# Kernel tuning notes

Hardware: AMD Instinct MI355X
Metric: run time of the kernel (lower is better)

## Reference

```python
import jax, jax.numpy as jnp
import numpy as np

N_CLUSTERS = 64
N_GHOST = 2
EPS = 1e-12  # F.normalize eps


def setup_inputs() -> dict:
    key = jax.random.key(0)
    k1, k2, k3, k4 = jax.random.split(key, 4)
    n_utts, feat_dim, duration = 16, 256, 1500
    x = jax.random.normal(k1, (n_utts, feat_dim, duration), dtype=jnp.float32)
    centroids = jax.random.uniform(k2, (N_CLUSTERS, feat_dim), dtype=jnp.float32)
    # NetVLAD init ties linear.weight = 2*alpha*centroids(+ghosts); here independent params suffice for a math baseline
    lin_w = jax.random.normal(k3, (N_CLUSTERS + N_GHOST, feat_dim), dtype=jnp.float32)
    lin_b = jax.random.normal(k4, (N_CLUSTERS + N_GHOST,), dtype=jnp.float32)
    return {"x": x, "centroids": centroids, "lin_w": lin_w, "lin_b": lin_b}


def reference(x, centroids, lin_w, lin_b):
    # x: [u, f, t] -> [u, t, f]
    n_utts = x.shape[0]
    xt = jnp.transpose(x, (0, 2, 1))
    # soft assignments over clusters+ghosts, then drop ghost columns
    logits = jnp.einsum('utf,cf->utc', xt, lin_w) + lin_b  # [u,t,C+G]
    a = jax.nn.softmax(logits, axis=2)[..., :N_CLUSTERS]   # [u,t,C]
    # Fused NetVLAD aggregation (algebraically identical to
    # sum_t a[u,t,c] * (x[u,t,:] - centroids[c,:]) without materializing
    # the [u,t,C,f] residual tensor):
    comp = jnp.einsum('utc,utf->ucf', a, xt) - a.sum(axis=1)[..., None] * centroids  # [u,C,f]
    # intra-normalization (F.normalize p=2 over feat dim)
    comp = comp / jnp.maximum(jnp.linalg.norm(comp, axis=2, keepdims=True), EPS)
    sv = comp.reshape(n_utts, -1)  # [u, C*f]
    sv = sv / jnp.maximum(jnp.linalg.norm(sv, axis=1, keepdims=True), EPS)
    return sv
```

## Files before the change

### kernel.cpp

```cpp
#include <hip/hip_runtime.h>
#include <math.h>


#define NU 16
#define NF 256
#define NT 1500
#define NC 64
#define NCG 66
#define EPSN 1e-12f
#define TCH 48
#define NCHUNK 32
#define XP 49

__device__ __forceinline__ float blk_reduce_sum(float v, float* sbuf) {
    #pragma unroll
    for (int off = 32; off > 0; off >>= 1) v += __shfl_down(v, off, 64);
    const int lane = threadIdx.x & 63, wv = threadIdx.x >> 6;
    if (lane == 0) sbuf[wv] = v;
    __syncthreads();
    float r = sbuf[0] + sbuf[1] + sbuf[2] + sbuf[3];
    __syncthreads();
    return r;
}

__global__ __launch_bounds__(256, 2) void ka_fused(
        const float* __restrict__ x, const float* __restrict__ lin_w,
        const float* __restrict__ lin_b, float* __restrict__ partial,
        float* __restrict__ asum_part) {
    __shared__ float Xsm[NF][XP];
    __shared__ float Asm[NC][XP];
    __shared__ float scratch[NCG * 64];

    const int chunk = blockIdx.x, u = blockIdx.y;
    const int tid = threadIdx.x, lane = tid & 63, wave = tid >> 6;
    const int t0 = chunk * TCH;

    {
        const int fr = tid >> 2;
        const int ks = (tid & 3) * 4;
        #pragma unroll
        for (int r = 0; r < 4; ++r) {
            const int f = fr + 64 * r;
            const float* rp = x + (size_t)(u * NF + f) * NT + t0;
            #pragma unroll
            for (int q = 0; q < 3; ++q) {
                const int kk = ks + 16 * q;
                const int tg = t0 + kk;
                float4 v;
                if (tg + 3 < NT) v = *(const float4*)(rp + kk);
                else {
                    v.x = (tg + 0 < NT) ? rp[kk + 0] : 0.0f;
                    v.y = (tg + 1 < NT) ? rp[kk + 1] : 0.0f;
                    v.z = (tg + 2 < NT) ? rp[kk + 2] : 0.0f;
                    v.w = (tg + 3 < NT) ? rp[kk + 3] : 0.0f;
                }
                Xsm[f][kk + 0] = v.x; Xsm[f][kk + 1] = v.y;
                Xsm[f][kk + 2] = v.z; Xsm[f][kk + 3] = v.w;
            }
        }
    }
    __syncthreads();

    float acc[NCG];
    #pragma unroll
    for (int c = 0; c < NCG; ++c) acc[c] = 0.0f;
    {
        const int kk = (lane < TCH) ? lane : (TCH - 1);
        float (*wsm)[NCG][16] = (float (*)[NCG][16])scratch;
        for (int fc = 0; fc < 4; ++fc) {
            const int fbase = wave * 64 + fc * 16;
            for (int idx = lane; idx < NCG * 16; idx += 64) {
                const int c = idx >> 4, k = idx & 15;
                wsm[wave][c][k] = lin_w[c * NF + fbase + k];
            }
            __syncthreads();
            float xv[16];
            #pragma unroll
            for (int k = 0; k < 16; ++k) xv[k] = Xsm[fbase + k][kk];
            #pragma unroll
            for (int c = 0; c < NCG; ++c) {
                const float4* wr = (const float4*)(&wsm[wave][c][0]);
                const float4 w0 = wr[0], w1 = wr[1], w2 = wr[2], w3 = wr[3];
                acc[c] += w0.x*xv[0]  + w0.y*xv[1]  + w0.z*xv[2]  + w0.w*xv[3]
                        + w1.x*xv[4]  + w1.y*xv[5]  + w1.z*xv[6]  + w1.w*xv[7]
                        + w2.x*xv[8]  + w2.y*xv[9]  + w2.z*xv[10] + w2.w*xv[11]
                        + w3.x*xv[12] + w3.y*xv[13] + w3.z*xv[14] + w3.w*xv[15];
            }
            __syncthreads();
        }
    }

    {
        float (*red)[64] = (float (*)[64])scratch;
        if (wave == 3) {
            #pragma unroll
            for (int c = 0; c < NCG; ++c) red[c][lane] = acc[c];
        }
        __syncthreads();
        if (wave == 1) {
            #pragma unroll
            for (int c = 0; c < NCG; ++c) acc[c] += red[c][lane];
        }
        __syncthreads();
        if (wave == 2) {
            #pragma unroll
            for (int c = 0; c < NCG; ++c) red[c][lane] = acc[c];
        }
        __syncthreads();
        if (wave == 0) {
            #pragma unroll
            for (int c = 0; c < NCG; ++c) acc[c] += red[c][lane];
        }
        __syncthreads();
        if (wave == 1) {
            #pragma unroll
            for (int c = 0; c < NCG; ++c) red[c][lane] = acc[c];
        }
        __syncthreads();
        if (wave == 0) {
            #pragma unroll
            for (int c = 0; c < NCG; ++c) acc[c] += red[c][lane] + lin_b[c];
            float m = -INFINITY;
            #pragma unroll
            for (int c = 0; c < NCG; ++c) m = fmaxf(m, acc[c]);
            float s = 0.0f;
            #pragma unroll
            for (int c = 0; c < NCG; ++c) { acc[c] = __expf(acc[c] - m); s += acc[c]; }
            const int t = t0 + lane;
            const float sc = (t < NT) ? (1.0f / s) : 0.0f;
            if (lane < TCH) {
                #pragma unroll
                for (int c = 0; c < NC; ++c) Asm[c][lane] = acc[c] * sc;
            }
        }
        __syncthreads();
    }

    {
        float ag[8][8], as[8];
        #pragma unroll
        for (int i = 0; i < 8; ++i) {
            as[i] = 0.0f;
            #pragma unroll
            for (int j = 0; j < 8; ++j) ag[i][j] = 0.0f;
        }
        const int cb = (tid >> 5) * 8;
        const int fl = tid & 31;

        #pragma unroll 4
        for (int k = 0; k < TCH; ++k) {
            float av[8], xv[8];
            #pragma unroll
            for (int i = 0; i < 8; ++i) av[i] = Asm[cb + i][k];
            #pragma unroll
            for (int j = 0; j < 8; ++j) xv[j] = Xsm[fl + 32 * j][k];
            #pragma unroll
            for (int i = 0; i < 8; ++i) {
                as[i] += av[i];
                #pragma unroll
                for (int j = 0; j < 8; ++j) ag[i][j] += av[i] * xv[j];
            }
        }

        #pragma unroll
        for (int i = 0; i < 8; ++i) {
            float* op = partial + ((size_t)((chunk * NU + u) * NC + cb + i)) * NF;
            #pragma unroll
            for (int j = 0; j < 8; ++j) op[fl + 32 * j] = ag[i][j];
        }
        if (fl == 0) {
            #pragma unroll
            for (int i = 0; i < 8; ++i)
                asum_part[(chunk * NU + u) * NC + cb + i] = as[i];
        }
    }
}

__global__ __launch_bounds__(256) void kb_norm(
        const float* __restrict__ asum_part, const float* __restrict__ partial,
        const float* __restrict__ centroids, float* __restrict__ compn,
        float* __restrict__ rowsq) {
    const int c = blockIdx.x, u = blockIdx.y;
    const int tid = threadIdx.x;
    __shared__ float sbuf[4];

    float asum = 0.0f;
    #pragma unroll
    for (int ch = 0; ch < NCHUNK; ++ch)
        asum += asum_part[(ch * NU + u) * NC + c];

    float val = 0.0f;
    #pragma unroll
    for (int ch = 0; ch < NCHUNK; ++ch)
        val += partial[((size_t)((ch * NU + u) * NC + c)) * NF + tid];
    val -= asum * centroids[c * NF + tid];

    const float ss = blk_reduce_sum(val * val, sbuf);
    const float d  = fmaxf(sqrtf(ss), EPSN);
    compn[((size_t)(u * NC + c)) * NF + tid] = val / d;
    if (tid == 0) rowsq[u * NC + c] = ss / (d * d);
}

__global__ __launch_bounds__(256) void kc_scale(
        const float* __restrict__ compn, const float* __restrict__ rowsq,
        float* __restrict__ out) {
    const int u = blockIdx.y, sl = blockIdx.x;
    const int tid = threadIdx.x;
    float g = 0.0f;
    #pragma unroll
    for (int c = 0; c < NC; ++c) g += rowsq[u * NC + c];
    const float inv = 1.0f / fmaxf(sqrtf(g), EPSN);
    const int base = u * (NC * NF) + sl * 1024 + tid * 4;
    float4 v = *(const float4*)(compn + base);
    v.x *= inv; v.y *= inv; v.z *= inv; v.w *= inv;
    *(float4*)(out + base) = v;
}

extern "C" void kernel_launch(void* const* d_in, const int* in_sizes, int n_in,
                              void* d_out, int out_size, void* d_ws, size_t ws_size,
                              hipStream_t stream) {
    (void)in_sizes; (void)n_in; (void)out_size; (void)ws_size;
    const float* x         = (const float*)d_in[0];
    const float* centroids = (const float*)d_in[1];
    const float* lin_w     = (const float*)d_in[2];
    const float* lin_b     = (const float*)d_in[3];
    float* out = (float*)d_out;

    float* ws        = (float*)d_ws;
    float* partial   = ws;
    float* asum_part = partial + (size_t)NCHUNK * NU * NC * NF;
    float* compn     = asum_part + NCHUNK * NU * NC;
    float* rowsq     = compn + (size_t)NU * NC * NF;

    dim3 blk(256);
    hipLaunchKernelGGL(ka_fused, dim3(NCHUNK, NU), blk, 0, stream,
                       x, lin_w, lin_b, partial, asum_part);
    hipLaunchKernelGGL(kb_norm,  dim3(NC, NU), blk, 0, stream,
                       asum_part, partial, centroids, compn, rowsq);
    hipLaunchKernelGGL(kc_scale, dim3(16, NU), blk, 0, stream,
                       compn, rowsq, out);
}
```

Measured before the change: 135.6 us.

## Double time chunk per block, read weights from global, retile aggregation

Doubles the time chunk per block to 96 and halves the chunk count, running 512 threads as two wave groups that each compute logits for part of the chunk. Weights are now read straight from global/cache instead of being staged through LDS with barriers. The aggregation is retiled to 8 clusters × 4 features per thread with float2 LDS reads. This halves the partial-sum traffic that the normalize kernel reduces. In exchange, LDS use grows to roughly 159KB, which limits each CU to one block, and half the lanes in the second group do redundant logit work.

```diff
diff --git a/kernel.cpp b/kernel.cpp
--- a/kernel.cpp
+++ b/kernel.cpp
@@ -8,9 +8,9 @@
 #define NC 64
 #define NCG 66
 #define EPSN 1e-12f
-#define TCH 48
-#define NCHUNK 32
-#define XP 49
+#define TCH 96
+#define NCHUNK 16
+#define XP 98
 
 __device__ __forceinline__ float blk_reduce_sum(float v, float* sbuf) {
     #pragma unroll
@@ -23,28 +23,30 @@
     return r;
 }
 
-__global__ __launch_bounds__(256, 2) void ka_fused(
+__global__ __launch_bounds__(512, 2) void ka_fused(
         const float* __restrict__ x, const float* __restrict__ lin_w,
         const float* __restrict__ lin_b, float* __restrict__ partial,
         float* __restrict__ asum_part) {
     __shared__ float Xsm[NF][XP];
     __shared__ float Asm[NC][XP];
-    __shared__ float scratch[NCG * 64];
+    __shared__ float red[2][NCG][64];
 
     const int chunk = blockIdx.x, u = blockIdx.y;
-    const int tid = threadIdx.x, lane = tid & 63, wave = tid >> 6;
+    const int tid  = threadIdx.x;
+    const int lane = tid & 63;
+    const int wave = tid >> 6;
     const int t0 = chunk * TCH;
 
     {
-        const int fr = tid >> 2;
-        const int ks = (tid & 3) * 4;
+        const int fr = tid >> 3;
+        const int ks = (tid & 7) * 4;
         #pragma unroll
         for (int r = 0; r < 4; ++r) {
             const int f = fr + 64 * r;
             const float* rp = x + (size_t)(u * NF + f) * NT + t0;
             #pragma unroll
             for (int q = 0; q < 3; ++q) {
-                const int kk = ks + 16 * q;
+                const int kk = ks + 32 * q;
                 const int tg = t0 + kk;
                 float4 v;
                 if (tg + 3 < NT) v = *(const float4*)(rp + kk);
@@ -54,111 +56,110 @@
                     v.z = (tg + 2 < NT) ? rp[kk + 2] : 0.0f;
                     v.w = (tg + 3 < NT) ? rp[kk + 3] : 0.0f;
                 }
-                Xsm[f][kk + 0] = v.x; Xsm[f][kk + 1] = v.y;
-                Xsm[f][kk + 2] = v.z; Xsm[f][kk + 3] = v.w;
+                *(float2*)&Xsm[f][kk]     = make_float2(v.x, v.y);
+                *(float2*)&Xsm[f][kk + 2] = make_float2(v.z, v.w);
             }
         }
     }
     __syncthreads();
 
+    const int grp  = wave >> 2;
+    const int wq   = __builtin_amdgcn_readfirstlane(wave & 3);
+    const int tcol = grp ? (64 + (lane & 31)) : lane;
+
     float acc[NCG];
     #pragma unroll
     for (int c = 0; c < NCG; ++c) acc[c] = 0.0f;
+
+    #pragma unroll
+    for (int fc = 0; fc < 4; ++fc) {
+        const int fbase = wq * 64 + fc * 16;
+        float xv[16];
+        #pragma unroll
+        for (int k = 0; k < 16; ++k) xv[k] = Xsm[fbase + k][tcol];
+        #pragma unroll
+        for (int c = 0; c < NCG; ++c) {
+            const float4* wp = (const float4*)(lin_w + c * NF + fbase);
+            const float4 w0 = wp[0], w1 = wp[1], w2 = wp[2], w3 = wp[3];
+            acc[c] += w0.x*xv[0]  + w0.y*xv[1]  + w0.z*xv[2]  + w0.w*xv[3]
+                    + w1.x*xv[4]  + w1.y*xv[5]  + w1.z*xv[6]  + w1.w*xv[7]
+                    + w2.x*xv[8]  + w2.y*xv[9]  + w2.z*xv[10] + w2.w*xv[11]
+                    + w3.x*xv[12] + w3.y*xv[13] + w3.z*xv[14] + w3.w*xv[15];
+        }
+    }
+
     {
-        const int kk = (lane < TCH) ? lane : (TCH - 1);
-        float (*wsm)[NCG][16] = (float (*)[NCG][16])scratch;
-        for (int fc = 0; fc < 4; ++fc) {
-            const int fbase = wave * 64 + fc * 16;
-            for (int idx = lane; idx < NCG * 16; idx += 64) {
-                const int c = idx >> 4, k = idx & 15;
-                wsm[wave][c][k] = lin_w[c * NF + fbase + k];
-            }
-            __syncthreads();
-            float xv[16];
-            #pragma unroll
-            for (int k = 0; k < 16; ++k) xv[k] = Xsm[fbase + k][kk];
-            #pragma unroll
-            for (int c = 0; c < NCG; ++c) {
-                const float4* wr = (const float4*)(&wsm[wave][c][0]);
-                const float4 w0 = wr[0], w1 = wr[1], w2 = wr[2], w3 = wr[3];
-                acc[c] += w0.x*xv[0]  + w0.y*xv[1]  + w0.z*xv[2]  + w0.w*xv[3]
-                        + w1.x*xv[4]  + w1.y*xv[5]  + w1.z*xv[6]  + w1.w*xv[7]
-                        + w2.x*xv[8]  + w2.y*xv[9]  + w2.z*xv[10] + w2.w*xv[11]
-                        + w3.x*xv[12] + w3.y*xv[13] + w3.z*xv[14] + w3.w*xv[15];
-            }
-            __syncthreads();
-        }
-    }
-
-    {
-        float (*red)[64] = (float (*)[64])scratch;
-        if (wave == 3) {
-            #pragma unroll
-            for (int c = 0; c < NCG; ++c) red[c][lane] = acc[c];
-        }
-        __syncthreads();
-        if (wave == 1) {
-            #pragma unroll
-            for (int c = 0; c < NCG; ++c) acc[c] += red[c][lane];
-        }
-        __syncthreads();
-        if (wave == 2) {
-            #pragma unroll
-            for (int c = 0; c < NCG; ++c) red[c][lane] = acc[c];
-        }
-        __syncthreads();
-        if (wave == 0) {
-            #pragma unroll
-            for (int c = 0; c < NCG; ++c) acc[c] += red[c][lane];
-        }
-        __syncthreads();
-        if (wave == 1) {
-            #pragma unroll
-            for (int c = 0; c < NCG; ++c) red[c][lane] = acc[c];
-        }
-        __syncthreads();
-        if (wave == 0) {
-            #pragma unroll
-            for (int c = 0; c < NCG; ++c) acc[c] += red[c][lane] + lin_b[c];
+        float (*redg)[64] = red[grp];
+        if (wq == 3) {
+            #pragma unroll
+            for (int c = 0; c < NCG; ++c) redg[c][lane] = acc[c];
+        }
+        __syncthreads();
+        if (wq == 1) {
+            #pragma unroll
+            for (int c = 0; c < NCG; ++c) acc[c] += redg[c][lane];
+        }
+        __syncthreads();
+        if (wq == 2) {
+            #pragma unroll
+            for (int c = 0; c < NCG; ++c) redg[c][lane] = acc[c];
+        }
+        __syncthreads();
+        if (wq == 0) {
+            #pragma unroll
+            for (int c = 0; c < NCG; ++c) acc[c] += redg[c][lane];
+        }
+        __syncthreads();
+        if (wq == 1) {
+            #pragma unroll
+            for (int c = 0; c < NCG; ++c) redg[c][lane] = acc[c];
+        }
+        __syncthreads();
+        if (wq == 0) {
+            #pragma unroll
+            for (int c = 0; c < NCG; ++c) acc[c] += redg[c][lane] + lin_b[c];
             float m = -INFINITY;
             #pragma unroll
             for (int c = 0; c < NCG; ++c) m = fmaxf(m, acc[c]);
             float s = 0.0f;
             #pragma unroll
             for (int c = 0; c < NCG; ++c) { acc[c] = __expf(acc[c] - m); s += acc[c]; }
-            const int t = t0 + lane;
+            const int t = t0 + tcol;
             const float sc = (t < NT) ? (1.0f / s) : 0.0f;
-            if (lane < TCH) {
+            if (grp == 0) {
                 #pragma unroll
                 for (int c = 0; c < NC; ++c) Asm[c][lane] = acc[c] * sc;
+            } else if (lane < 32) {
+                #pragma unroll
+                for (int c = 0; c < NC; ++c) Asm[c][64 + lane] = acc[c] * sc;
             }
         }
         __syncthreads();
     }
 
     {
-        float ag[8][8], as[8];
+        const int cb = wave * 8;
+        float ag[8][4], as[8];
         #pragma unroll
         for (int i = 0; i < 8; ++i) {
             as[i] = 0.0f;
             #pragma unroll
-            for (int j = 0; j < 8; ++j) ag[i][j] = 0.0f;
-        }
-        const int cb = (tid >> 5) * 8;
-        const int fl = tid & 31;
+            for (int j = 0; j < 4; ++j) ag[i][j] = 0.0f;
+        }
 
         #pragma unroll 4
-        for (int k = 0; k < TCH; ++k) {
-            float av[8], xv[8];
-            #pragma unroll
-            for (int i = 0; i < 8; ++i) av[i] = Asm[cb + i][k];
-            #pragma unroll
-            for (int j = 0; j < 8; ++j) xv[j] = Xsm[fl + 32 * j][k];
+        for (int k = 0; k < TCH; k += 2) {
+            float2 av[8], xv2[4];
+            #pragma unroll
+            for (int i = 0; i < 8; ++i) av[i] = *(const float2*)&Asm[cb + i][k];
+            #pragma unroll
+            for (int j = 0; j < 4; ++j) xv2[j] = *(const float2*)&Xsm[lane + 64 * j][k];
             #pragma unroll
             for (int i = 0; i < 8; ++i) {
-                as[i] += av[i];
+                as[i] += av[i].x + av[i].y;
                 #pragma unroll
-                for (int j = 0; j < 8; ++j) ag[i][j] += av[i] * xv[j];
+                for (int j = 0; j < 4; ++j)
+                    ag[i][j] += av[i].x * xv2[j].x + av[i].y * xv2[j].y;
             }
         }
 
@@ -166,9 +167,9 @@
         for (int i = 0; i < 8; ++i) {
             float* op = partial + ((size_t)((chunk * NU + u) * NC + cb + i)) * NF;
             #pragma unroll
-            for (int j = 0; j < 8; ++j) op[fl + 32 * j] = ag[i][j];
-        }
-        if (fl == 0) {
+            for (int j = 0; j < 4; ++j) op[lane + 64 * j] = ag[i][j];
+        }
+        if (lane == 0) {
             #pragma unroll
             for (int i = 0; i < 8; ++i)
                 asum_part[(chunk * NU + u) * NC + cb + i] = as[i];
@@ -232,11 +233,10 @@
     float* compn     = asum_part + NCHUNK * NU * NC;
     float* rowsq     = compn + (size_t)NU * NC * NF;
 
-    dim3 blk(256);
-    hipLaunchKernelGGL(ka_fused, dim3(NCHUNK, NU), blk, 0, stream,
+    hipLaunchKernelGGL(ka_fused, dim3(NCHUNK, NU), dim3(512), 0, stream,
                        x, lin_w, lin_b, partial, asum_part);
-    hipLaunchKernelGGL(kb_norm,  dim3(NC, NU), blk, 0, stream,
+    hipLaunchKernelGGL(kb_norm,  dim3(NC, NU), dim3(256), 0, stream,
                        asum_part, partial, centroids, compn, rowsq);
-    hipLaunchKernelGGL(kc_scale, dim3(16, NU), blk, 0, stream,
+    hipLaunchKernelGGL(kc_scale, dim3(16, NU), dim3(256), 0, stream,
                        compn, rowsq, out);
 }
```

Measured after the change: 152.4 us. 12.4% more time.

## Read lin_w directly from global in logits loop and vectorize per-wave norm kernel

Applied to the files above, without the earlier changes.

The logits stage no longer stages lin_w chunks through shared memory with two block barriers per feature chunk. Each thread now reads float4 weights straight from global memory, with an asm zero offset that forces per-lane vector loads instead of scalar loads. The norm kernel now gives each wave one cluster row, using float4 loads and a wave-level shuffle reduction in place of the block-level reduction. This cuts barriers and launched blocks, but adds redundant global/L1 weight traffic in the hot loop.

```diff
diff --git a/kernel.cpp b/kernel.cpp
--- a/kernel.cpp
+++ b/kernel.cpp
@@ -12,24 +12,13 @@
 #define NCHUNK 32
 #define XP 49
 
-__device__ __forceinline__ float blk_reduce_sum(float v, float* sbuf) {
-    #pragma unroll
-    for (int off = 32; off > 0; off >>= 1) v += __shfl_down(v, off, 64);
-    const int lane = threadIdx.x & 63, wv = threadIdx.x >> 6;
-    if (lane == 0) sbuf[wv] = v;
-    __syncthreads();
-    float r = sbuf[0] + sbuf[1] + sbuf[2] + sbuf[3];
-    __syncthreads();
-    return r;
-}
-
 __global__ __launch_bounds__(256, 2) void ka_fused(
         const float* __restrict__ x, const float* __restrict__ lin_w,
         const float* __restrict__ lin_b, float* __restrict__ partial,
         float* __restrict__ asum_part) {
     __shared__ float Xsm[NF][XP];
     __shared__ float Asm[NC][XP];
-    __shared__ float scratch[NCG * 64];
+    __shared__ float red[NCG][64];
 
     const int chunk = blockIdx.x, u = blockIdx.y;
     const int tid = threadIdx.x, lane = tid & 63, wave = tid >> 6;
@@ -65,33 +54,28 @@
     #pragma unroll
     for (int c = 0; c < NCG; ++c) acc[c] = 0.0f;
     {
+        int vzero;
+        asm volatile("v_mov_b32 %0, 0" : "=v"(vzero));
         const int kk = (lane < TCH) ? lane : (TCH - 1);
-        float (*wsm)[NCG][16] = (float (*)[NCG][16])scratch;
         for (int fc = 0; fc < 4; ++fc) {
             const int fbase = wave * 64 + fc * 16;
-            for (int idx = lane; idx < NCG * 16; idx += 64) {
-                const int c = idx >> 4, k = idx & 15;
-                wsm[wave][c][k] = lin_w[c * NF + fbase + k];
-            }
-            __syncthreads();
+            const float* wb = lin_w + fbase + vzero;
             float xv[16];
             #pragma unroll
             for (int k = 0; k < 16; ++k) xv[k] = Xsm[fbase + k][kk];
             #pragma unroll
             for (int c = 0; c < NCG; ++c) {
-                const float4* wr = (const float4*)(&wsm[wave][c][0]);
-                const float4 w0 = wr[0], w1 = wr[1], w2 = wr[2], w3 = wr[3];
+                const float4* wp = (const float4*)(wb + c * NF);
+                const float4 w0 = wp[0], w1 = wp[1], w2 = wp[2], w3 = wp[3];
                 acc[c] += w0.x*xv[0]  + w0.y*xv[1]  + w0.z*xv[2]  + w0.w*xv[3]
                         + w1.x*xv[4]  + w1.y*xv[5]  + w1.z*xv[6]  + w1.w*xv[7]
                         + w2.x*xv[8]  + w2.y*xv[9]  + w2.z*xv[10] + w2.w*xv[11]
                         + w3.x*xv[12] + w3.y*xv[13] + w3.z*xv[14] + w3.w*xv[15];
             }
-            __syncthreads();
-        }
-    }
-
-    {
-        float (*red)[64] = (float (*)[64])scratch;
+        }
+    }
+
+    {
         if (wave == 3) {
             #pragma unroll
             for (int c = 0; c < NCG; ++c) red[c][lane] = acc[c];
@@ -180,25 +164,37 @@
         const float* __restrict__ asum_part, const float* __restrict__ partial,
         const float* __restrict__ centroids, float* __restrict__ compn,
         float* __restrict__ rowsq) {
-    const int c = blockIdx.x, u = blockIdx.y;
-    const int tid = threadIdx.x;
-    __shared__ float sbuf[4];
+    const int u = blockIdx.y;
+    const int wave = threadIdx.x >> 6, lane = threadIdx.x & 63;
+    const int c = blockIdx.x * 4 + wave;
 
     float asum = 0.0f;
     #pragma unroll
     for (int ch = 0; ch < NCHUNK; ++ch)
         asum += asum_part[(ch * NU + u) * NC + c];
 
-    float val = 0.0f;
-    #pragma unroll
-    for (int ch = 0; ch < NCHUNK; ++ch)
-        val += partial[((size_t)((ch * NU + u) * NC + c)) * NF + tid];
-    val -= asum * centroids[c * NF + tid];
-
-    const float ss = blk_reduce_sum(val * val, sbuf);
-    const float d  = fmaxf(sqrtf(ss), EPSN);
-    compn[((size_t)(u * NC + c)) * NF + tid] = val / d;
-    if (tid == 0) rowsq[u * NC + c] = ss / (d * d);
+    float4 val = make_float4(0.f, 0.f, 0.f, 0.f);
+    #pragma unroll 8
+    for (int ch = 0; ch < NCHUNK; ++ch) {
+        const float4 p = *(const float4*)(
+            partial + ((size_t)((ch * NU + u) * NC + c)) * NF + lane * 4);
+        val.x += p.x; val.y += p.y; val.z += p.z; val.w += p.w;
+    }
+    const float4 ce = *(const float4*)(centroids + c * NF + lane * 4);
+    val.x -= asum * ce.x; val.y -= asum * ce.y;
+    val.z -= asum * ce.z; val.w -= asum * ce.w;
+
+    float ss = val.x * val.x + val.y * val.y + val.z * val.z + val.w * val.w;
+    #pragma unroll
+    for (int off = 32; off > 0; off >>= 1) ss += __shfl_down(ss, off, 64);
+    ss = __shfl(ss, 0, 64);
+
+    const float d   = fmaxf(sqrtf(ss), EPSN);
+    const float inv = 1.0f / d;
+    float4 o;
+    o.x = val.x * inv; o.y = val.y * inv; o.z = val.z * inv; o.w = val.w * inv;
+    *(float4*)(compn + ((size_t)(u * NC + c)) * NF + lane * 4) = o;
+    if (lane == 0) rowsq[u * NC + c] = ss / (d * d);
 }
 
 __global__ __launch_bounds__(256) void kc_scale(
@@ -235,7 +231,7 @@
     dim3 blk(256);
     hipLaunchKernelGGL(ka_fused, dim3(NCHUNK, NU), blk, 0, stream,
                        x, lin_w, lin_b, partial, asum_part);
-    hipLaunchKernelGGL(kb_norm,  dim3(NC, NU), blk, 0, stream,
+    hipLaunchKernelGGL(kb_norm,  dim3(16, NU), blk, 0, stream,
                        asum_part, partial, centroids, compn, rowsq);
     hipLaunchKernelGGL(kc_scale, dim3(16, NU), blk, 0, stream,
                        compn, rowsq, out);
```

New measurement: 165.3 us. 1.22x slower.
